# Optimization experiments

Measured on AMD Instinct MI355X. Metric: run time of the kernel, lower is better.

## Reference

```python
import jax, jax.numpy as jnp
import numpy as np
from jax import lax

PRED_LEN = 48  # prediction_length


def setup_inputs() -> dict:
    key = jax.random.key(0)
    ks = jax.random.split(key, 7)
    B, T, IN, H, OUT = 1024, 512, 1, 512, 1
    s = 1.0 / float(np.sqrt(H))  # PyTorch default uniform init bound
    x = jax.random.normal(ks[0], (B, T, IN), dtype=jnp.float32)
    w_ih = jax.random.uniform(ks[1], (4 * H, IN), jnp.float32, -s, s)
    w_hh = jax.random.uniform(ks[2], (4 * H, H), jnp.float32, -s, s)
    b_ih = jax.random.uniform(ks[3], (4 * H,), jnp.float32, -s, s)
    b_hh = jax.random.uniform(ks[4], (4 * H,), jnp.float32, -s, s)
    w_fc = jax.random.uniform(ks[5], (OUT, H), jnp.float32, -s, s)
    b_fc = jax.random.uniform(ks[6], (OUT,), jnp.float32, -s, s)
    return {"x": x, "w_ih": w_ih, "w_hh": w_hh, "b_ih": b_ih,
            "b_hh": b_hh, "w_fc": w_fc, "b_fc": b_fc}


def _lstm_cell(xt, h, c, w_ih, w_hh, b):
    # PyTorch gate order: input, forget, cell(g), output
    g = xt @ w_ih.T + h @ w_hh.T + b  # [B, 4H]
    i, f, gg, o = jnp.split(g, 4, axis=-1)
    c = jax.nn.sigmoid(f) * c + jax.nn.sigmoid(i) * jnp.tanh(gg)
    h = jax.nn.sigmoid(o) * jnp.tanh(c)
    return h, c


def reference(x, w_ih, w_hh, b_ih, b_hh, w_fc, b_fc):
    B = x.shape[0]
    H = w_hh.shape[1]
    b = b_ih + b_hh
    h0 = jnp.zeros((B, H), x.dtype)
    c0 = jnp.zeros((B, H), x.dtype)

    # --- encoder: full-sequence LSTM over x, batch_first -> scan over time ---
    def enc_step(carry, xt):
        h, c = carry
        h, c = _lstm_cell(xt, h, c, w_ih, w_hh, b)
        return (h, c), None

    (h, c), _ = lax.scan(enc_step, (h0, c0), jnp.swapaxes(x, 0, 1))

    def dec_step(carry, _):
        h, c = carry
        out = h @ w_fc.T + b_fc  # dropout is identity at inference
        h, c = _lstm_cell(out, h, c, w_ih, w_hh, b)
        return (h, c), out

    _, preds = lax.scan(dec_step, (h, c), None, length=PRED_LEN)  # [P, B, OUT]
    return jnp.swapaxes(preds, 0, 1)  # [B, P, OUT]
```

## Files before the change

### kernel.cpp

```cpp
#include <hip/hip_runtime.h>

typedef _Float16 f16x8 __attribute__((ext_vector_type(8)));
typedef float    f32x4 __attribute__((ext_vector_type(4)));
typedef unsigned long long u64;
typedef u64 u64x2 __attribute__((ext_vector_type(2)));

constexpr int BATCH = 1024;
constexpr int HDIM  = 512;
constexpr int TENC  = 512;
constexpr int PRED  = 48;
constexpr int STEPS = TENC + PRED - 1;
constexpr int NG    = 64;
constexpr int GB    = 16;
constexpr int UBU   = 64;
constexpr int HB_OFF = 32768;

constexpr u64 TAG_MASK = 0x0001000100010001ull;
__device__ __forceinline__ u64 tag_of(int t) {
  return ((u64)(t & 1) | ((u64)((t >> 1) & 1) << 16)) * 0x0000000100000001ull;
}

__global__ void init_kernel(int* wsi) {
  int idx = blockIdx.x * blockDim.x + threadIdx.x;
  int stride = gridDim.x * blockDim.x;
  const int nws = (HB_OFF + BATCH * HDIM * 2) / 4;
  for (int i = idx; i < nws; i += stride) wsi[i] = 0;
}

static __device__ __forceinline__ f16x8 load16_llc(const _Float16* p) {
  f16x8 v;
  asm volatile("global_load_dwordx4 %0, %1, off sc0 sc1"
               : "=v"(v) : "v"((u64)p) : "memory");
  return v;
}
static __device__ __forceinline__ unsigned loadc_llc(const void* p) {
  unsigned v;
  asm volatile("global_load_dword %0, %1, off sc0 sc1"
               : "=v"(v) : "v"((u64)p) : "memory");
  return v;
}
static __device__ __forceinline__ float loadx(const float* p) {
  float v;
  asm volatile("global_load_dword %0, %1, off"
               : "=v"(v) : "v"((u64)p) : "memory");
  return v;
}
static __device__ __forceinline__ void sleep_bk(int stage) {
  if (stage == 0)      __builtin_amdgcn_s_sleep(1);
  else if (stage == 1) __builtin_amdgcn_s_sleep(2);
  else if (stage == 2) __builtin_amdgcn_s_sleep(4);
  else                 __builtin_amdgcn_s_sleep(8);
}
static __device__ __forceinline__ void wait_vm0_fenced() {
  asm volatile("s_waitcnt vmcnt(0)" ::: "memory");
  __builtin_amdgcn_sched_barrier(0);
}
static __device__ __forceinline__ void wait_vm1_fenced() {
  asm volatile("s_waitcnt vmcnt(1)" ::: "memory");
  __builtin_amdgcn_sched_barrier(0);
}
static __device__ __forceinline__ void lds_barrier() {
  asm volatile("s_waitcnt lgkmcnt(0)" ::: "memory");
  __builtin_amdgcn_s_barrier();
}

__global__ __launch_bounds__(512, 2) void lstm_persist(
    const float* __restrict__ x,
    const float* __restrict__ w_ih,
    const float* __restrict__ w_hh,
    const float* __restrict__ b_ih,
    const float* __restrict__ b_hh,
    const float* __restrict__ w_fc,
    const float* __restrict__ b_fc,
    float* __restrict__ out,
    _Float16* __restrict__ hbuf)
{
  const int bid  = blockIdx.x;
  const int gA   = bid >> 3;
  const int ub   = bid & 7;
  const int tid  = threadIdx.x;
  const int wid  = tid >> 6;
  const int ws   = wid >> 2;
  const int wq   = wid & 3;
  const int lane = tid & 63;
  const int quad = lane >> 4;
  const int lcol = lane & 15;
  const int bA0  = gA * GB;
  const int bB0  = bA0 + NG / 2 * GB;
  const int myu  = ub * UBU + wq * 16 + lcol;
  const int cb   = tid >> 5;
  const int cu   = (tid * 2) & 63;

  __shared__ __align__(16) _Float16 hsA[GB][520];
  __shared__ __align__(16) _Float16 hsB[GB][520];
  __shared__ __align__(16) _Float16 wz[520];
  __shared__ float gl[4][GB][68];
  __shared__ float xls[GB];
  __shared__ float outs[2][GB][PRED];

  wz[tid < 512 ? tid : 0] = (_Float16)w_fc[tid < 512 ? tid : 0];
  if (tid < 8) wz[512 + tid] = (_Float16)0.f;

  f16x8 wf2[2][16];
#pragma unroll
  for (int ntl = 0; ntl < 2; ++ntl) {
    const int j = (2 * ws + ntl) * HDIM + myu;
#pragma unroll
    for (int kc = 0; kc < 16; ++kc) {
      const float* s = w_hh + (size_t)j * HDIM + kc * 32 + quad * 8;
      f16x8 v;
#pragma unroll
      for (int i = 0; i < 8; ++i) v[i] = (_Float16)s[i];
      wf2[ntl][kc] = v;
    }
  }
  float wihc[2][4], biasc[2][4];
#pragma unroll
  for (int e = 0; e < 2; ++e)
#pragma unroll
    for (int g = 0; g < 4; ++g) {
      const int j = g * HDIM + ub * UBU + cu + e;
      wihc[e][g]  = w_ih[j];
      biasc[e][g] = b_ih[j] + b_hh[j];
    }
  const float bfc = b_fc[0];

  float cstA2[2] = {0.f, 0.f}, cstB2[2] = {0.f, 0.f};
  f16x8 tA[2], tB[2];
  float xA, xB;

  auto issue2 = [&](f16x8* tr, const _Float16* base) {
#pragma unroll
    for (int i = 0; i < 2; ++i) {
      const int c = i * 512 + tid;
      tr[i] = load16_llc(base + (size_t)(c >> 6) * HDIM + (c & 63) * 8);
    }
  };
  auto validate2 = [&](f16x8* tr, const _Float16* base, u64 expect) {
    const unsigned exp32 = (unsigned)expect & 0x00010001u;
    unsigned stale = 0;
#pragma unroll
    for (int i = 0; i < 2; ++i) {
      u64x2 w2 = __builtin_bit_cast(u64x2, tr[i]);
      if (((w2[0] & TAG_MASK) != expect) || ((w2[1] & TAG_MASK) != expect))
        stale |= 1u << i;
    }
    int slp = 0;
    while (stale) {
      sleep_bk(slp);
      if (slp < 3) ++slp;
      unsigned cv[2];
#pragma unroll
      for (int i = 0; i < 2; ++i)
        if (stale & (1u << i)) {
          const int c = i * 512 + tid;
          cv[i] = loadc_llc(base + (size_t)(c >> 6) * HDIM + (c & 63) * 8);
        }
      wait_vm0_fenced();
      unsigned rdy = 0;
#pragma unroll
      for (int i = 0; i < 2; ++i)
        if ((stale & (1u << i)) && ((cv[i] & 0x00010001u) == exp32))
          rdy |= 1u << i;
      if (!rdy) continue;
#pragma unroll
      for (int i = 0; i < 2; ++i)
        if (rdy & (1u << i)) {
          const int c = i * 512 + tid;
          tr[i] = load16_llc(base + (size_t)(c >> 6) * HDIM + (c & 63) * 8);
        }
      wait_vm0_fenced();
#pragma unroll
      for (int i = 0; i < 2; ++i)
        if (rdy & (1u << i)) {
          u64x2 w2 = __builtin_bit_cast(u64x2, tr[i]);
          if (((w2[0] & TAG_MASK) == expect) && ((w2[1] & TAG_MASK) == expect))
            stale &= ~(1u << i);
        }
    }
  };
  auto stage2 = [&](f16x8* tr, _Float16 (*hsp)[520]) {
#pragma unroll
    for (int i = 0; i < 2; ++i) {
      const int c = i * 512 + tid;
      *reinterpret_cast<f16x8*>(&hsp[c >> 6][(c & 63) * 8]) = tr[i];
    }
  };
  auto gemm2 = [&](const _Float16 (*hsp)[520], f32x4* acc, f32x4& accF, bool dec) {
#pragma unroll
    for (int kc = 0; kc < 16; ++kc) {
      const f16x8 a = *reinterpret_cast<const f16x8*>(&hsp[lcol][kc * 32 + quad * 8]);
      acc[0] = __builtin_amdgcn_mfma_f32_16x16x32_f16(a, wf2[0][kc], acc[0], 0, 0, 0);
      acc[1] = __builtin_amdgcn_mfma_f32_16x16x32_f16(a, wf2[1][kc], acc[1], 0, 0, 0);
      if (dec && ws == 0) {
        const f16x8 wv = *reinterpret_cast<const f16x8*>(
            &wz[(lcol == 0) ? (kc * 32 + quad * 8) : 512]);
        accF = __builtin_amdgcn_mfma_f32_16x16x32_f16(a, wv, accF, 0, 0, 0);
      }
    }
  };
  auto phase_epi = [&](f32x4* acc, f32x4& accF, float xreg, float* cstv,
                       int bX0, int gidx, int t, _Float16* hnxt, bool dec) {
#pragma unroll
    for (int ntl = 0; ntl < 2; ++ntl)
#pragma unroll
      for (int r = 0; r < 4; ++r)
        gl[2 * ws + ntl][quad * 4 + r][wq * 16 + lcol] = acc[ntl][r];
    if (dec && wid == 0 && lcol == 0) {
#pragma unroll
      for (int r = 0; r < 4; ++r) xls[quad * 4 + r] = accF[r] + bfc;
    }
    lds_barrier();
    if (dec && ub == 0 && (tid & 31) == 0)
      outs[gidx][cb][t - TENC] = xls[cb];
    const float xt = dec ? xls[cb] : xreg;
    if (t < STEPS) {
      const unsigned tag32 = (unsigned)tag_of(t + 1);
      unsigned v32 = 0;
#pragma unroll
      for (int e = 0; e < 2; ++e) {
        const int u = cu + e;
        const float gi = gl[0][cb][u] + xt * wihc[e][0] + biasc[e][0];
        const float gf = gl[1][cb][u] + xt * wihc[e][1] + biasc[e][1];
        const float gg = gl[2][cb][u] + xt * wihc[e][2] + biasc[e][2];
        const float go = gl[3][cb][u] + xt * wihc[e][3] + biasc[e][3];
        const float si = 1.f / (1.f + __expf(-gi));
        const float sf = 1.f / (1.f + __expf(-gf));
        const float so = 1.f / (1.f + __expf(-go));
        const float tg = 1.f - 2.f / (1.f + __expf(2.f * gg));
        const float cn = sf * cstv[e] + si * tg;
        cstv[e] = cn;
        const float tc = 1.f - 2.f / (1.f + __expf(2.f * cn));
        const unsigned short hb =
            __builtin_bit_cast(unsigned short, (_Float16)(so * tc));
        v32 |= ((unsigned)hb) << (16 * e);
      }
      v32 = (v32 & ~0x00010001u) | tag32;
      unsigned* dst = (unsigned*)(hnxt + (size_t)(bX0 + cb) * HDIM
                                  + ub * UBU + cu);
      __hip_atomic_store(dst, v32, __ATOMIC_RELAXED, __HIP_MEMORY_SCOPE_AGENT);
    }
  };

  lds_barrier();

  issue2(tA, hbuf + (size_t)bA0 * HDIM);
  xA = loadx(x + (size_t)(bA0 + cb) * TENC + 0);

  for (int t = 0; t <= STEPS; ++t) {
    const _Float16* hcur = hbuf + (size_t)(t & 1) * BATCH * HDIM;
    _Float16*       hnxt = hbuf + (size_t)((t + 1) & 1) * BATCH * HDIM;
    const u64 expect = tag_of(t);
    const bool dec = (t >= TENC);

    if (t == 0) wait_vm0_fenced();
    else        wait_vm1_fenced();
    asm volatile("" :: "v"(xA));
    validate2(tA, hcur + (size_t)bA0 * HDIM, expect);
    stage2(tA, hsA);
    lds_barrier();
    issue2(tB, hcur + (size_t)bB0 * HDIM);
    xB = loadx(x + (size_t)(bB0 + cb) * TENC + (t < TENC ? t : TENC - 1));

    f32x4 accA[2], accFA;
    accA[0] = (f32x4){0.f, 0.f, 0.f, 0.f};
    accA[1] = (f32x4){0.f, 0.f, 0.f, 0.f};
    accFA = (f32x4){0.f, 0.f, 0.f, 0.f};
    gemm2(hsA, accA, accFA, dec);
    phase_epi(accA, accFA, xA, cstA2, bA0, 0, t, hnxt, dec);

    if (t == STEPS) wait_vm0_fenced();
    else            wait_vm1_fenced();
    asm volatile("" :: "v"(xB));
    validate2(tB, hcur + (size_t)bB0 * HDIM, expect);
    stage2(tB, hsB);
    lds_barrier();
    if (t < STEPS) {
      issue2(tA, hnxt + (size_t)bA0 * HDIM);
      xA = loadx(x + (size_t)(bA0 + cb) * TENC
                 + (t + 1 < TENC ? t + 1 : TENC - 1));
    }

    f32x4 accB[2], accFB;
    accB[0] = (f32x4){0.f, 0.f, 0.f, 0.f};
    accB[1] = (f32x4){0.f, 0.f, 0.f, 0.f};
    accFB = (f32x4){0.f, 0.f, 0.f, 0.f};
    gemm2(hsB, accB, accFB, dec);
    phase_epi(accB, accFB, xB, cstB2, bB0, 1, t, hnxt, dec);
  }

  lds_barrier();
  if (ub == 0) {
    for (int k = tid; k < 2 * GB * PRED; k += 512) {
      const int g  = k / (GB * PRED);
      const int rm = k % (GB * PRED);
      out[(size_t)((g ? bB0 : bA0) + rm / PRED) * PRED + (rm % PRED)] =
          outs[g][rm / PRED][rm % PRED];
    }
  }
}

extern "C" void kernel_launch(void* const* d_in, const int* in_sizes, int n_in,
                              void* d_out, int out_size, void* d_ws, size_t ws_size,
                              hipStream_t stream) {
  const float* x    = (const float*)d_in[0];
  const float* w_ih = (const float*)d_in[1];
  const float* w_hh = (const float*)d_in[2];
  const float* b_ih = (const float*)d_in[3];
  const float* b_hh = (const float*)d_in[4];
  const float* w_fc = (const float*)d_in[5];
  const float* b_fc = (const float*)d_in[6];
  float* out = (float*)d_out;
  _Float16* hbuf = (_Float16*)((char*)d_ws + HB_OFF);

  hipLaunchKernelGGL(init_kernel, dim3(256), dim3(256), 0, stream, (int*)d_ws);
  hipLaunchKernelGGL(lstm_persist, dim3(256), dim3(512), 0, stream,
                     x, w_ih, w_hh, b_ih, b_hh, w_fc, b_fc, out, hbuf);
}
```

Before: 2.652 ms.

## Split ping-pong batch groups across twice as many persistent blocks

Result: slower. 8.086 ms (+204.9%).

```diff
diff --git a/kernel.cpp b/kernel.cpp
--- a/kernel.cpp
+++ b/kernel.cpp
@@ -55,16 +55,12 @@
   asm volatile("s_waitcnt vmcnt(0)" ::: "memory");
   __builtin_amdgcn_sched_barrier(0);
 }
-static __device__ __forceinline__ void wait_vm1_fenced() {
-  asm volatile("s_waitcnt vmcnt(1)" ::: "memory");
-  __builtin_amdgcn_sched_barrier(0);
-}
 static __device__ __forceinline__ void lds_barrier() {
   asm volatile("s_waitcnt lgkmcnt(0)" ::: "memory");
   __builtin_amdgcn_s_barrier();
 }
 
-__global__ __launch_bounds__(512, 2) void lstm_persist(
+__global__ __launch_bounds__(512, 4) void lstm_persist(
     const float* __restrict__ x,
     const float* __restrict__ w_ih,
     const float* __restrict__ w_hh,
@@ -76,7 +72,7 @@
     _Float16* __restrict__ hbuf)
 {
   const int bid  = blockIdx.x;
-  const int gA   = bid >> 3;
+  const int grp  = bid >> 3;
   const int ub   = bid & 7;
   const int tid  = threadIdx.x;
   const int wid  = tid >> 6;
@@ -85,20 +81,18 @@
   const int lane = tid & 63;
   const int quad = lane >> 4;
   const int lcol = lane & 15;
-  const int bA0  = gA * GB;
-  const int bB0  = bA0 + NG / 2 * GB;
+  const int b0   = grp * GB;
   const int myu  = ub * UBU + wq * 16 + lcol;
   const int cb   = tid >> 5;
   const int cu   = (tid * 2) & 63;
 
-  __shared__ __align__(16) _Float16 hsA[GB][520];
-  __shared__ __align__(16) _Float16 hsB[GB][520];
+  __shared__ __align__(16) _Float16 hs[GB][520];
   __shared__ __align__(16) _Float16 wz[520];
   __shared__ float gl[4][GB][68];
   __shared__ float xls[GB];
-  __shared__ float outs[2][GB][PRED];
-
-  wz[tid < 512 ? tid : 0] = (_Float16)w_fc[tid < 512 ? tid : 0];
+  __shared__ float outs[GB][PRED];
+
+  wz[tid] = (tid < 512) ? (_Float16)w_fc[tid] : (_Float16)0.f;
   if (tid < 8) wz[512 + tid] = (_Float16)0.f;
 
   f16x8 wf2[2][16];
@@ -125,9 +119,9 @@
     }
   const float bfc = b_fc[0];
 
-  float cstA2[2] = {0.f, 0.f}, cstB2[2] = {0.f, 0.f};
-  f16x8 tA[2], tB[2];
-  float xA, xB;
+  float cst2[2] = {0.f, 0.f};
+  f16x8 tA[2];
+  float xA;
 
   auto issue2 = [&](f16x8* tr, const _Float16* base) {
 #pragma unroll
@@ -179,17 +173,17 @@
         }
     }
   };
-  auto stage2 = [&](f16x8* tr, _Float16 (*hsp)[520]) {
+  auto stage2 = [&](f16x8* tr) {
 #pragma unroll
     for (int i = 0; i < 2; ++i) {
       const int c = i * 512 + tid;
-      *reinterpret_cast<f16x8*>(&hsp[c >> 6][(c & 63) * 8]) = tr[i];
-    }
-  };
-  auto gemm2 = [&](const _Float16 (*hsp)[520], f32x4* acc, f32x4& accF, bool dec) {
+      *reinterpret_cast<f16x8*>(&hs[c >> 6][(c & 63) * 8]) = tr[i];
+    }
+  };
+  auto gemm2 = [&](f32x4* acc, f32x4& accF, bool dec) {
 #pragma unroll
     for (int kc = 0; kc < 16; ++kc) {
-      const f16x8 a = *reinterpret_cast<const f16x8*>(&hsp[lcol][kc * 32 + quad * 8]);
+      const f16x8 a = *reinterpret_cast<const f16x8*>(&hs[lcol][kc * 32 + quad * 8]);
       acc[0] = __builtin_amdgcn_mfma_f32_16x16x32_f16(a, wf2[0][kc], acc[0], 0, 0, 0);
       acc[1] = __builtin_amdgcn_mfma_f32_16x16x32_f16(a, wf2[1][kc], acc[1], 0, 0, 0);
       if (dec && ws == 0) {
@@ -199,8 +193,8 @@
       }
     }
   };
-  auto phase_epi = [&](f32x4* acc, f32x4& accF, float xreg, float* cstv,
-                       int bX0, int gidx, int t, _Float16* hnxt, bool dec) {
+  auto phase_epi = [&](f32x4* acc, f32x4& accF, float xreg,
+                       int t, _Float16* hnxt, bool dec) {
 #pragma unroll
     for (int ntl = 0; ntl < 2; ++ntl)
 #pragma unroll
@@ -212,7 +206,7 @@
     }
     lds_barrier();
     if (dec && ub == 0 && (tid & 31) == 0)
-      outs[gidx][cb][t - TENC] = xls[cb];
+      outs[cb][t - TENC] = xls[cb];
     const float xt = dec ? xls[cb] : xreg;
     if (t < STEPS) {
       const unsigned tag32 = (unsigned)tag_of(t + 1);
@@ -228,15 +222,15 @@
         const float sf = 1.f / (1.f + __expf(-gf));
         const float so = 1.f / (1.f + __expf(-go));
         const float tg = 1.f - 2.f / (1.f + __expf(2.f * gg));
-        const float cn = sf * cstv[e] + si * tg;
-        cstv[e] = cn;
+        const float cn = sf * cst2[e] + si * tg;
+        cst2[e] = cn;
         const float tc = 1.f - 2.f / (1.f + __expf(2.f * cn));
         const unsigned short hb =
             __builtin_bit_cast(unsigned short, (_Float16)(so * tc));
         v32 |= ((unsigned)hb) << (16 * e);
       }
       v32 = (v32 & ~0x00010001u) | tag32;
-      unsigned* dst = (unsigned*)(hnxt + (size_t)(bX0 + cb) * HDIM
+      unsigned* dst = (unsigned*)(hnxt + (size_t)(b0 + cb) * HDIM
                                   + ub * UBU + cu);
       __hip_atomic_store(dst, v32, __ATOMIC_RELAXED, __HIP_MEMORY_SCOPE_AGENT);
     }
@@ -244,8 +238,8 @@
 
   lds_barrier();
 
-  issue2(tA, hbuf + (size_t)bA0 * HDIM);
-  xA = loadx(x + (size_t)(bA0 + cb) * TENC + 0);
+  issue2(tA, hbuf + (size_t)b0 * HDIM);
+  xA = loadx(x + (size_t)(b0 + cb) * TENC + 0);
 
   for (int t = 0; t <= STEPS; ++t) {
     const _Float16* hcur = hbuf + (size_t)(t & 1) * BATCH * HDIM;
@@ -253,50 +247,30 @@
     const u64 expect = tag_of(t);
     const bool dec = (t >= TENC);
 
-    if (t == 0) wait_vm0_fenced();
-    else        wait_vm1_fenced();
+    wait_vm0_fenced();
     asm volatile("" :: "v"(xA));
-    validate2(tA, hcur + (size_t)bA0 * HDIM, expect);
-    stage2(tA, hsA);
+    validate2(tA, hcur + (size_t)b0 * HDIM, expect);
+    stage2(tA);
     lds_barrier();
-    issue2(tB, hcur + (size_t)bB0 * HDIM);
-    xB = loadx(x + (size_t)(bB0 + cb) * TENC + (t < TENC ? t : TENC - 1));
-
-    f32x4 accA[2], accFA;
-    accA[0] = (f32x4){0.f, 0.f, 0.f, 0.f};
-    accA[1] = (f32x4){0.f, 0.f, 0.f, 0.f};
-    accFA = (f32x4){0.f, 0.f, 0.f, 0.f};
-    gemm2(hsA, accA, accFA, dec);
-    phase_epi(accA, accFA, xA, cstA2, bA0, 0, t, hnxt, dec);
-
-    if (t == STEPS) wait_vm0_fenced();
-    else            wait_vm1_fenced();
-    asm volatile("" :: "v"(xB));
-    validate2(tB, hcur + (size_t)bB0 * HDIM, expect);
-    stage2(tB, hsB);
-    lds_barrier();
+
+    f32x4 acc[2], accF;
+    acc[0] = (f32x4){0.f, 0.f, 0.f, 0.f};
+    acc[1] = (f32x4){0.f, 0.f, 0.f, 0.f};
+    accF = (f32x4){0.f, 0.f, 0.f, 0.f};
+    gemm2(acc, accF, dec);
+    phase_epi(acc, accF, xA, t, hnxt, dec);
+
     if (t < STEPS) {
-      issue2(tA, hnxt + (size_t)bA0 * HDIM);
-      xA = loadx(x + (size_t)(bA0 + cb) * TENC
+      issue2(tA, hnxt + (size_t)b0 * HDIM);
+      xA = loadx(x + (size_t)(b0 + cb) * TENC
                  + (t + 1 < TENC ? t + 1 : TENC - 1));
     }
-
-    f32x4 accB[2], accFB;
-    accB[0] = (f32x4){0.f, 0.f, 0.f, 0.f};
-    accB[1] = (f32x4){0.f, 0.f, 0.f, 0.f};
-    accFB = (f32x4){0.f, 0.f, 0.f, 0.f};
-    gemm2(hsB, accB, accFB, dec);
-    phase_epi(accB, accFB, xB, cstB2, bB0, 1, t, hnxt, dec);
   }
 
   lds_barrier();
   if (ub == 0) {
-    for (int k = tid; k < 2 * GB * PRED; k += 512) {
-      const int g  = k / (GB * PRED);
-      const int rm = k % (GB * PRED);
-      out[(size_t)((g ? bB0 : bA0) + rm / PRED) * PRED + (rm % PRED)] =
-          outs[g][rm / PRED][rm % PRED];
-    }
+    for (int k = tid; k < GB * PRED; k += 512)
+      out[(size_t)(b0 + k / PRED) * PRED + (k % PRED)] = outs[k / PRED][k % PRED];
   }
 }
 
@@ -314,6 +288,6 @@
   _Float16* hbuf = (_Float16*)((char*)d_ws + HB_OFF);
 
   hipLaunchKernelGGL(init_kernel, dim3(256), dim3(256), 0, stream, (int*)d_ws);
-  hipLaunchKernelGGL(lstm_persist, dim3(256), dim3(512), 0, stream,
+  hipLaunchKernelGGL(lstm_persist, dim3(512), dim3(512), 0, stream,
                      x, w_ih, w_hh, b_ih, b_hh, w_fc, b_fc, out, hbuf);
 }
```
